# Performance work log

Hardware: AMD Instinct MI355X
Metric: run time of the kernel (lower is better)

Reference implementation:

```python
import jax, jax.numpy as jnp
import numpy as np

N_NODES = 50000
N_EDGES = 800000
IN_DIM = 256
HID = 64
HEADS = [4, 4, 1]
N_CLASSES = 16
SLOPE = 0.2


def mish(x):
    return x * jnp.tanh(jax.nn.softplus(x))


def gat_conv(x, src, dst, W, attn_l, attn_r, bias, res_W, n_heads, d_out, act):
    """DGL GATConv (feat_drop=attn_drop=0, residual=True, bias=True).
    x: (N, F_in); src/dst: (E,) edge endpoints; message flows src -> dst.
    """
    N = x.shape[0]
    feat = (x @ W).reshape(N, n_heads, d_out)            # (N, H, D)
    el = jnp.sum(feat * attn_l, axis=-1)                 # (N, H)
    er = jnp.sum(feat * attn_r, axis=-1)                 # (N, H)
    e = jax.nn.leaky_relu(el[src] + er[dst], SLOPE)      # (E, H)
    # segment softmax over incoming edges of each dst node
    emax = jax.ops.segment_max(e, dst, num_segments=N)   # (N, H)
    ee = jnp.exp(e - emax[dst])                          # (E, H)
    denom = jax.ops.segment_sum(ee, dst, num_segments=N) # (N, H)
    a = ee / denom[dst]                                  # (E, H)
    # weighted scatter-aggregate of source features
    rst = jax.ops.segment_sum(feat[src] * a[:, :, None], dst, num_segments=N)  # (N, H, D)
    # residual: identity if F_in == H*D else linear projection (DGL semantics)
    if res_W is None:
        res = x.reshape(N, n_heads, d_out)
    else:
        res = (x @ res_W).reshape(N, n_heads, d_out)
    rst = rst + res + bias.reshape(1, n_heads, d_out)
    if act:
        rst = mish(rst)
    return rst


def setup_inputs() -> dict:
    key = jax.random.key(0)
    ks = jax.random.split(key, 16)
    x = jax.random.normal(ks[0], (N_NODES, IN_DIM), dtype=jnp.float32)
    src = jax.random.randint(ks[1], (N_EDGES,), 0, N_NODES, dtype=jnp.int32)
    dst = jax.random.randint(ks[2], (N_EDGES,), 0, N_NODES, dtype=jnp.int32)
    s = 0.1
    # layer 0: 256 -> 4 heads x 64
    W0 = jax.random.normal(ks[3], (IN_DIM, HEADS[0] * HID), jnp.float32) * s
    al0 = jax.random.normal(ks[4], (HEADS[0], HID), jnp.float32) * s
    ar0 = jax.random.normal(ks[5], (HEADS[0], HID), jnp.float32) * s
    b0 = jnp.zeros((HEADS[0] * HID,), jnp.float32)
    # layer 1: 256 -> 4 heads x 64
    W1 = jax.random.normal(ks[6], (HEADS[0] * HID, HEADS[1] * HID), jnp.float32) * s
    al1 = jax.random.normal(ks[7], (HEADS[1], HID), jnp.float32) * s
    ar1 = jax.random.normal(ks[8], (HEADS[1], HID), jnp.float32) * s
    b1 = jnp.zeros((HEADS[1] * HID,), jnp.float32)
    # output layer: 256 -> 1 head x 16 (residual needs a linear projection)
    W2 = jax.random.normal(ks[9], (HEADS[1] * HID, HEADS[2] * N_CLASSES), jnp.float32) * s
    al2 = jax.random.normal(ks[10], (HEADS[2], N_CLASSES), jnp.float32) * s
    ar2 = jax.random.normal(ks[11], (HEADS[2], N_CLASSES), jnp.float32) * s
    b2 = jnp.zeros((HEADS[2] * N_CLASSES,), jnp.float32)
    resW2 = jax.random.normal(ks[12], (HEADS[1] * HID, HEADS[2] * N_CLASSES), jnp.float32) * s
    return {"x": x, "src": src, "dst": dst,
            "W0": W0, "al0": al0, "ar0": ar0, "b0": b0,
            "W1": W1, "al1": al1, "ar1": ar1, "b1": b1,
            "W2": W2, "al2": al2, "ar2": ar2, "b2": b2, "resW2": resW2}


def reference(x, src, dst, W0, al0, ar0, b0, W1, al1, ar1, b1, W2, al2, ar2, b2, resW2):
    N = x.shape[0]
    h = gat_conv(x, src, dst, W0, al0, ar0, b0, None, HEADS[0], HID, True).reshape(N, -1)
    h = gat_conv(h, src, dst, W1, al1, ar1, b1, None, HEADS[1], HID, True).reshape(N, -1)
    logits = gat_conv(h, src, dst, W2, al2, ar2, b2, resW2, HEADS[2], N_CLASSES, False).mean(axis=1)
    return logits
```

## Files before the change

### kernel.cpp

```cpp
#include <hip/hip_runtime.h>
#include <cmath>
#include <type_traits>

typedef __bf16 bf16;
typedef __attribute__((ext_vector_type(8))) __bf16 bf16x8;
typedef __attribute__((ext_vector_type(4))) __bf16 bf16x4;
typedef __attribute__((ext_vector_type(4))) float f32x4;

__device__ __forceinline__ unsigned f2s(float x) {
    unsigned u = __float_as_uint(x);
    return (u & 0x80000000u) ? ~u : (u | 0x80000000u);
}
__device__ __forceinline__ float s2f(unsigned s) {
    return (s & 0x80000000u) ? __uint_as_float(s & 0x7FFFFFFFu)
                             : __uint_as_float(~s);
}

__device__ __forceinline__ float fast_mish(float x) {
    const float t = __expf(fminf(x, 32.f));
    const float num = fmaf(t, t, t + t);
    const float den = num + 2.f;
    return x * num * __builtin_amdgcn_rcpf(den);
}

__global__ void prep_weights_kernel(const float* __restrict__ W0, const float* __restrict__ W1,
                                    const float* __restrict__ W2, const float* __restrict__ rW2,
                                    bf16* __restrict__ Wt0, bf16* __restrict__ Wt1,
                                    bf16* __restrict__ Bct) {
    const int idx = blockIdx.x * blockDim.x + threadIdx.x;
    if (idx < 65536) {
        const int k = idx >> 8, m = idx & 255;
        Wt0[m * 256 + k] = (bf16)W0[idx];
        Wt1[m * 256 + k] = (bf16)W1[idx];
    }
    if (idx < 8192) {
        const int m = idx >> 8, k = idx & 255;
        const float v = (m < 16) ? W2[k * 16 + m] : rW2[k * 16 + (m - 16)];
        Bct[idx] = (bf16)v;
    }
}

template <typename AT>
__global__ __launch_bounds__(256) void gemm_mfma_bf16(const AT* __restrict__ A,
                                                      const bf16* __restrict__ Bt,
                                                      bf16* __restrict__ Fb, int N) {
    constexpr int K = 256, BM = 128, BK = 32;
    constexpr int LDA = BK + 8;
    __shared__ bf16 As[BM * LDA];
    __shared__ bf16 Bs[BM * LDA];

    const int tid = threadIdx.x;
    const int wave = tid >> 6, lane = tid & 63;
    const int quad = lane >> 4, l16 = lane & 15;
    const int rowBase = blockIdx.y * BM;
    const int colBase = blockIdx.x * BM;
    const int m_base = (wave >> 1) * 64, n_base = (wave & 1) * 64;

    f32x4 acc[4][4] = {};

    const int sr = tid >> 1;
    const int seg = (tid & 1) << 4;

    for (int k0 = 0; k0 < K; k0 += BK) {
        {
            const int gr = rowBase + sr;
            if constexpr (std::is_same<AT, float>::value) {
                float4 f0 = {0,0,0,0}, f1 = {0,0,0,0}, f2 = {0,0,0,0}, f3 = {0,0,0,0};
                if (gr < N) {
                    const float4* Ag = (const float4*)(A + (long)gr * K + k0 + seg);
                    f0 = Ag[0]; f1 = Ag[1]; f2 = Ag[2]; f3 = Ag[3];
                }
                bf16x8 p0, p1;
                p0[0] = (bf16)f0.x; p0[1] = (bf16)f0.y; p0[2] = (bf16)f0.z; p0[3] = (bf16)f0.w;
                p0[4] = (bf16)f1.x; p0[5] = (bf16)f1.y; p0[6] = (bf16)f1.z; p0[7] = (bf16)f1.w;
                p1[0] = (bf16)f2.x; p1[1] = (bf16)f2.y; p1[2] = (bf16)f2.z; p1[3] = (bf16)f2.w;
                p1[4] = (bf16)f3.x; p1[5] = (bf16)f3.y; p1[6] = (bf16)f3.z; p1[7] = (bf16)f3.w;
                *(bf16x8*)&As[sr * LDA + seg] = p0;
                *(bf16x8*)&As[sr * LDA + seg + 8] = p1;
            } else {
                bf16x8 p0 = {}, p1 = {};
                if (gr < N) {
                    const bf16x8* Ag = (const bf16x8*)(A + (long)gr * K + k0 + seg);
                    p0 = Ag[0]; p1 = Ag[1];
                }
                *(bf16x8*)&As[sr * LDA + seg] = p0;
                *(bf16x8*)&As[sr * LDA + seg + 8] = p1;
            }
        }
        {
            const bf16x8* Bg = (const bf16x8*)(Bt + (long)(colBase + sr) * K + k0 + seg);
            *(bf16x8*)&Bs[sr * LDA + seg] = Bg[0];
            *(bf16x8*)&Bs[sr * LDA + seg + 8] = Bg[1];
        }
        __syncthreads();

        bf16x8 af[4], bfr[4];
#pragma unroll
        for (int mi = 0; mi < 4; mi++)
            af[mi] = *(const bf16x8*)&As[(m_base + mi * 16 + l16) * LDA + quad * 8];
#pragma unroll
        for (int ni = 0; ni < 4; ni++)
            bfr[ni] = *(const bf16x8*)&Bs[(n_base + ni * 16 + l16) * LDA + quad * 8];
#pragma unroll
        for (int mi = 0; mi < 4; mi++)
#pragma unroll
            for (int ni = 0; ni < 4; ni++)
                acc[mi][ni] = __builtin_amdgcn_mfma_f32_16x16x32_bf16(af[mi], bfr[ni], acc[mi][ni], 0, 0, 0);
        __syncthreads();
    }

#pragma unroll
    for (int mi = 0; mi < 4; mi++) {
#pragma unroll
        for (int r = 0; r < 4; r++) {
            const int grow = rowBase + m_base + mi * 16 + quad * 4 + r;
            if (grow < N) {
#pragma unroll
                for (int ni = 0; ni < 4; ni++) {
                    Fb[(long)grow * 256 + colBase + n_base + ni * 16 + l16] = (bf16)acc[mi][ni][r];
                }
            }
        }
    }
}

__global__ __launch_bounds__(256) void gemm_mfma_n32(const bf16* __restrict__ A,
                                                     const bf16* __restrict__ Bt,
                                                     float* __restrict__ C, int N) {
    constexpr int K = 256, BM = 128, BK = 32;
    constexpr int LDA = BK + 8;
    __shared__ bf16 As[BM * LDA];
    __shared__ bf16 Bs[32 * LDA];

    const int tid = threadIdx.x;
    const int wave = tid >> 6, lane = tid & 63;
    const int quad = lane >> 4, l16 = lane & 15;
    const int rowBase = blockIdx.x * BM;
    const int m_base = (wave >> 1) * 64, n_base = (wave & 1) * 16;

    f32x4 acc[4] = {};

    const int sr = tid >> 1;
    const int seg = (tid & 1) << 4;

    for (int k0 = 0; k0 < K; k0 += BK) {
        {
            const int gr = rowBase + sr;
            bf16x8 p0 = {}, p1 = {};
            if (gr < N) {
                const bf16x8* Ag = (const bf16x8*)(A + (long)gr * K + k0 + seg);
                p0 = Ag[0]; p1 = Ag[1];
            }
            *(bf16x8*)&As[sr * LDA + seg] = p0;
            *(bf16x8*)&As[sr * LDA + seg + 8] = p1;
        }
        if (tid < 64) {
            const int br = tid >> 1;
            const bf16x8* Bg = (const bf16x8*)(Bt + br * K + k0 + seg);
            *(bf16x8*)&Bs[br * LDA + seg] = Bg[0];
            *(bf16x8*)&Bs[br * LDA + seg + 8] = Bg[1];
        }
        __syncthreads();

        const bf16x8 bfr = *(const bf16x8*)&Bs[(n_base + l16) * LDA + quad * 8];
#pragma unroll
        for (int mi = 0; mi < 4; mi++) {
            const bf16x8 af = *(const bf16x8*)&As[(m_base + mi * 16 + l16) * LDA + quad * 8];
            acc[mi] = __builtin_amdgcn_mfma_f32_16x16x32_bf16(af, bfr, acc[mi], 0, 0, 0);
        }
        __syncthreads();
    }

#pragma unroll
    for (int mi = 0; mi < 4; mi++) {
#pragma unroll
        for (int r = 0; r < 4; r++) {
            const int grow = rowBase + m_base + mi * 16 + quad * 4 + r;
            if (grow < N) C[(long)grow * 32 + n_base + l16] = acc[mi][r];
        }
    }
}

__global__ void el_er_node_kernel(const bf16* __restrict__ feat,
                                  const float* __restrict__ al, const float* __restrict__ ar,
                                  float* __restrict__ el, float* __restrict__ er, int N) {
    const int wid = (blockIdx.x * blockDim.x + threadIdx.x) >> 6;
    const int lane = threadIdx.x & 63;
    if (wid >= N) return;
    const bf16x4 f = ((const bf16x4*)feat)[(long)wid * 64 + lane];
    const float4 a = ((const float4*)al)[lane];
    const float4 b = ((const float4*)ar)[lane];
    const float f0 = (float)f[0], f1 = (float)f[1], f2 = (float)f[2], f3 = (float)f[3];
    float vl = f0 * a.x + f1 * a.y + f2 * a.z + f3 * a.w;
    float vr = f0 * b.x + f1 * b.y + f2 * b.z + f3 * b.w;
#pragma unroll
    for (int off = 1; off < 16; off <<= 1) {
        vl += __shfl_xor(vl, off);
        vr += __shfl_xor(vr, off);
    }
    if ((lane & 15) == 0) {
        const int h = lane >> 4;
        el[wid * 4 + h] = vl;
        er[wid * 4 + h] = vr;
    }
}

__global__ void el_er_strided16(const float* __restrict__ feat, int stride,
                                const float* __restrict__ al, const float* __restrict__ ar,
                                float* __restrict__ el, float* __restrict__ er, int N) {
    const int wid = (blockIdx.x * blockDim.x + threadIdx.x) >> 6;
    const int lane = threadIdx.x & 63;
    if (wid >= N) return;
    float vl = 0.f, vr = 0.f;
    if (lane < 16) {
        float f = feat[(long)wid * stride + lane];
        vl = f * al[lane];
        vr = f * ar[lane];
    }
#pragma unroll
    for (int off = 1; off < 16; off <<= 1) {
        vl += __shfl_xor(vl, off);
        vr += __shfl_xor(vr, off);
    }
    if (lane == 0) { el[wid] = vl; er[wid] = vr; }
}

__global__ void elmax4_kernel(const float4* __restrict__ el4, unsigned* __restrict__ elmax_u, int n4) {
    __shared__ float4 sm[256];
    float4 m = {-INFINITY, -INFINITY, -INFINITY, -INFINITY};
    for (int i = blockIdx.x * blockDim.x + threadIdx.x; i < n4; i += gridDim.x * blockDim.x) {
        const float4 v = el4[i];
        m.x = fmaxf(m.x, v.x); m.y = fmaxf(m.y, v.y);
        m.z = fmaxf(m.z, v.z); m.w = fmaxf(m.w, v.w);
    }
    sm[threadIdx.x] = m;
    __syncthreads();
    for (int off = 128; off > 0; off >>= 1) {
        if (threadIdx.x < off) {
            float4 o = sm[threadIdx.x + off];
            float4 c = sm[threadIdx.x];
            c.x = fmaxf(c.x, o.x); c.y = fmaxf(c.y, o.y);
            c.z = fmaxf(c.z, o.z); c.w = fmaxf(c.w, o.w);
            sm[threadIdx.x] = c;
        }
        __syncthreads();
    }
    if (threadIdx.x == 0) {
        const float4 r = sm[0];
        atomicMax(&elmax_u[0], f2s(r.x));
        atomicMax(&elmax_u[1], f2s(r.y));
        atomicMax(&elmax_u[2], f2s(r.z));
        atomicMax(&elmax_u[3], f2s(r.w));
    }
}


__global__ void count_deg_kernel(const int* __restrict__ dst, int* __restrict__ deg, int E) {
    const int e = blockIdx.x * blockDim.x + threadIdx.x;
    if (e >= E) return;
    atomicAdd(&deg[dst[e]], 1);
}

__global__ void scan_block_kernel(const int* __restrict__ deg, int* __restrict__ scanned,
                                  int* __restrict__ block_sums, int N) {
    __shared__ int smem[256];
    const int tid = threadIdx.x;
    const int base = blockIdx.x * 1024 + tid * 4;
    int v[4];
#pragma unroll
    for (int i = 0; i < 4; i++) v[i] = (base + i < N) ? deg[base + i] : 0;
    const int tsum = v[0] + v[1] + v[2] + v[3];
    smem[tid] = tsum;
    __syncthreads();
    int acc = tsum;
    for (int off = 1; off < 256; off <<= 1) {
        const int t = (tid >= off) ? smem[tid - off] : 0;
        __syncthreads();
        acc += t;
        smem[tid] = acc;
        __syncthreads();
    }
    if (tid == 255) block_sums[blockIdx.x] = acc;
    int run = acc - tsum;
#pragma unroll
    for (int i = 0; i < 4; i++) {
        if (base + i < N) scanned[base + i] = run;
        run += v[i];
    }
}

__global__ void scan_sums_kernel(int* __restrict__ block_sums, unsigned* __restrict__ elmax_u, int nb) {
    const int tid = threadIdx.x;
    if (tid < 12) elmax_u[tid] = f2s(-INFINITY);
    const int orig = (tid < nb) ? block_sums[tid] : 0;
    int v = orig;
#pragma unroll
    for (int off = 1; off < 64; off <<= 1) {
        const int t = __shfl_up(v, off);
        if (tid >= off) v += t;
    }
    if (tid < nb) block_sums[tid] = v - orig;
}

__global__ void apply_offsets_kernel(const int* __restrict__ scanned, const int* __restrict__ block_sums,
                                     int* __restrict__ row_ptr, int* __restrict__ cursor, int N, int E) {
    const int i = blockIdx.x * blockDim.x + threadIdx.x;
    if (i < N) {
        const int v = scanned[i] + block_sums[i >> 10];
        row_ptr[i] = v;
        cursor[i] = v;
    }
    if (i == 0) row_ptr[N] = E;
}

__global__ void scatter_kernel(const int* __restrict__ src, const int* __restrict__ dst,
                               int* __restrict__ cursor, int* __restrict__ csr_src, int E) {
    const int e = blockIdx.x * blockDim.x + threadIdx.x;
    if (e >= E) return;
    const int pos = atomicAdd(&cursor[dst[e]], 1);
    csr_src[pos] = src[e];
}

template <int H, int D, bool ACT, typename RT, typename OT>
__global__ void gat_aggregate_wave(const int* __restrict__ row_ptr, const int* __restrict__ csr_src,
                                   const float* __restrict__ el, const float* __restrict__ er,
                                   const unsigned* __restrict__ elmax_u,
                                   const bf16* __restrict__ feat,
                                   const RT* __restrict__ res, const float* __restrict__ bias,
                                   OT* __restrict__ out, int N) {
    static_assert(H == 4 && D == 64, "layout hardcoded for C=256");
    const int wave = threadIdx.x >> 6;
    const int lane = threadIdx.x & 63;
    int n = blockIdx.x * (blockDim.x >> 6) + wave;
    if (n >= N) return;
    n = __builtin_amdgcn_readfirstlane(n);
    const int sel = lane >> 5;
    const int hl = lane & 31;
    const int h = hl >> 3;

    const float erd = er[n * H + h];
    float sh = s2f(elmax_u[h]) + erd;
    sh = fmaxf(sh, 0.2f * sh);
    constexpr float L2E = 1.4426950408889634f;
    const float C1 = (erd - sh) * L2E;
    const float C2 = fmaf(0.2f, erd, -sh) * L2E;

    const char* csrB = (const char*)csr_src;
    const char* elB = (const char*)el;
    const char* featB = (const char*)feat;
    const unsigned hoff = (unsigned)(h << 2);
    const unsigned coff = (unsigned)(hl << 4);
    const unsigned selo = (unsigned)(sel << 2);

    float acc[8] = {0.f, 0.f, 0.f, 0.f, 0.f, 0.f, 0.f, 0.f};
    float l = 0.f;
    int p = row_ptr[n];
    const int pend = row_ptr[n + 1];

#define CSRLD(PP) (*(const int*)(csrB + ((unsigned)((PP) << 2) + selo)))
#define ELLD(S)   (*(const float*)(elB + ((unsigned)((S) << 4) + hoff)))
#define FTLD(S)   (*(const bf16x8*)(featB + ((unsigned)((S) << 9) + coff)))
#define WCOMP(EV) __builtin_amdgcn_exp2f(fmaxf(fmaf((EV), L2E, C1), fmaf((EV), 0.2f * L2E, C2)))

    for (; p + 8 <= pend; p += 8) {
        const int sA = CSRLD(p);
        const int sB = CSRLD(p + 2);
        const int sC = CSRLD(p + 4);
        const int sD = CSRLD(p + 6);
        const float eA = ELLD(sA);
        const float eB = ELLD(sB);
        const float eC = ELLD(sC);
        const float eD = ELLD(sD);
        const bf16x8 fA = FTLD(sA);
        const bf16x8 fB = FTLD(sB);
        const bf16x8 fC = FTLD(sC);
        const bf16x8 fD = FTLD(sD);
        const float wA = WCOMP(eA);
        const float wB = WCOMP(eB);
        const float wC = WCOMP(eC);
        const float wD = WCOMP(eD);
        l += (wA + wB) + (wC + wD);
#pragma unroll
        for (int i = 0; i < 8; i++)
            acc[i] = fmaf(wA, (float)fA[i],
                     fmaf(wB, (float)fB[i],
                     fmaf(wC, (float)fC[i],
                     fmaf(wD, (float)fD[i], acc[i]))));
    }
    for (; p + 4 <= pend; p += 4) {
        const int sA = CSRLD(p);
        const int sB = CSRLD(p + 2);
        const float eA = ELLD(sA);
        const float eB = ELLD(sB);
        const bf16x8 fA = FTLD(sA);
        const bf16x8 fB = FTLD(sB);
        const float wA = WCOMP(eA);
        const float wB = WCOMP(eB);
        l += wA + wB;
#pragma unroll
        for (int i = 0; i < 8; i++)
            acc[i] = fmaf(wA, (float)fA[i], fmaf(wB, (float)fB[i], acc[i]));
    }
    for (; p + 2 <= pend; p += 2) {
        const int sA = CSRLD(p);
        const float eA = ELLD(sA);
        const bf16x8 fA = FTLD(sA);
        const float wA = WCOMP(eA);
        l += wA;
#pragma unroll
        for (int i = 0; i < 8; i++)
            acc[i] = fmaf(wA, (float)fA[i], acc[i]);
    }
    if (p < pend) {
        const int s_ = *(const int*)(csrB + (unsigned)(p << 2));
        const float ev_ = ELLD(s_);
        float w_ = WCOMP(ev_);
        if (sel) w_ = 0.f;
        const bf16x8 f_ = FTLD(s_);
        l += w_;
#pragma unroll
        for (int i_ = 0; i_ < 8; i_++) acc[i_] = fmaf(w_, (float)f_[i_], acc[i_]);
    }
#undef CSRLD
#undef ELLD
#undef FTLD
#undef WCOMP

    l += __shfl_xor(l, 32);
#pragma unroll
    for (int i = 0; i < 8; i++) acc[i] += __shfl_xor(acc[i], 32);
    const float inv = (l > 0.f) ? __builtin_amdgcn_rcpf(l) : 0.f;

    const float a0 = (sel ? acc[4] : acc[0]) * inv;
    const float a1 = (sel ? acc[5] : acc[1]) * inv;
    const float a2 = (sel ? acc[6] : acc[2]) * inv;
    const float a3 = (sel ? acc[7] : acc[3]) * inv;
    const unsigned ib = (unsigned)(sel << 2);

    float4 r;
    if constexpr (std::is_same<RT, float>::value) {
        r = *(const float4*)((const char*)res + ((size_t)n << 10) + (coff << 1) + (ib << 2));
    } else {
        const bf16x4 rb = *(const bf16x4*)((const char*)res + ((size_t)n << 9) + coff + (ib << 1));
        r = make_float4((float)rb[0], (float)rb[1], (float)rb[2], (float)rb[3]);
    }
    const float4 bb = *(const float4*)((const char*)bias + (coff << 1) + (ib << 2));
    float v0 = a0 + r.x + bb.x;
    float v1 = a1 + r.y + bb.y;
    float v2 = a2 + r.z + bb.z;
    float v3 = a3 + r.w + bb.w;
    if (ACT) {
        v0 = fast_mish(v0);
        v1 = fast_mish(v1);
        v2 = fast_mish(v2);
        v3 = fast_mish(v3);
    }
    if constexpr (std::is_same<OT, float>::value) {
        float4 o = {v0, v1, v2, v3};
        *(float4*)((char*)out + ((size_t)n << 10) + (coff << 1) + (ib << 2)) = o;
    } else {
        bf16x4 o;
        o[0] = (bf16)v0; o[1] = (bf16)v1; o[2] = (bf16)v2; o[3] = (bf16)v3;
        *(bf16x4*)((char*)out + ((size_t)n << 9) + coff + (ib << 1)) = o;
    }
}

__global__ void gat_aggregate_small16(const int* __restrict__ row_ptr, const int* __restrict__ csr_src,
                                      const float* __restrict__ el, const float* __restrict__ er,
                                      const unsigned* __restrict__ elmax_u,
                                      const float* __restrict__ F2, const float* __restrict__ bias,
                                      float* __restrict__ out, int N) {
    const int wave = threadIdx.x >> 6;
    const int lane = threadIdx.x & 63;
    int n = blockIdx.x * (blockDim.x >> 6) + wave;
    if (n >= N) return;
    n = __builtin_amdgcn_readfirstlane(n);
    const int slot = lane >> 4;
    const int c = lane & 15;

    const float mx = fmaxf(fmaxf(s2f(elmax_u[8]), s2f(elmax_u[9])),
                           fmaxf(s2f(elmax_u[10]), s2f(elmax_u[11])));
    const float erd = er[n];
    float sh = mx + erd;
    sh = fmaxf(sh, 0.2f * sh);
    constexpr float L2E = 1.4426950408889634f;
    const float C1 = (erd - sh) * L2E;
    const float C2 = fmaf(0.2f, erd, -sh) * L2E;

    const char* csrB = (const char*)csr_src;
    const char* elB = (const char*)el;
    const char* fB = (const char*)F2;
    const unsigned co = (unsigned)(c << 2);
    const unsigned so = (unsigned)(slot << 2);

    float acc = 0.f, l = 0.f;
    int p = row_ptr[n];
    const int pend = row_ptr[n + 1];
    for (; p + 8 <= pend; p += 8) {
        const int s0 = *(const int*)(csrB + ((unsigned)(p << 2) + so));
        const int s1 = *(const int*)(csrB + ((unsigned)((p + 4) << 2) + so));
        const float e0 = *(const float*)(elB + (unsigned)(s0 << 2));
        const float e1 = *(const float*)(elB + (unsigned)(s1 << 2));
        const float f0 = *(const float*)(fB + ((unsigned)(s0 << 7) + co));
        const float f1 = *(const float*)(fB + ((unsigned)(s1 << 7) + co));
        const float w0 = __builtin_amdgcn_exp2f(
            fmaxf(fmaf(e0, L2E, C1), fmaf(e0, 0.2f * L2E, C2)));
        const float w1 = __builtin_amdgcn_exp2f(
            fmaxf(fmaf(e1, L2E, C1), fmaf(e1, 0.2f * L2E, C2)));
        l += w0 + w1;
        acc = fmaf(w0, f0, fmaf(w1, f1, acc));
    }
    for (; p + 4 <= pend; p += 4) {
        const int s_ = *(const int*)(csrB + ((unsigned)(p << 2) + so));
        const float ev_ = *(const float*)(elB + (unsigned)(s_ << 2));
        const float w_ = __builtin_amdgcn_exp2f(
            fmaxf(fmaf(ev_, L2E, C1), fmaf(ev_, 0.2f * L2E, C2)));
        const float f_ = *(const float*)(fB + ((unsigned)(s_ << 7) + co));
        l += w_;
        acc = fmaf(w_, f_, acc);
    }
    if (p < pend) {
        const int q = p + slot;
        const bool valid = q < pend;
        const int qi = valid ? q : p;
        const int s_ = *(const int*)(csrB + (unsigned)(qi << 2));
        const float ev_ = *(const float*)(elB + (unsigned)(s_ << 2));
        float w_ = __builtin_amdgcn_exp2f(
            fmaxf(fmaf(ev_, L2E, C1), fmaf(ev_, 0.2f * L2E, C2)));
        if (!valid) w_ = 0.f;
        const float f_ = *(const float*)(fB + ((unsigned)(s_ << 7) + co));
        l += w_;
        acc = fmaf(w_, f_, acc);
    }
    l += __shfl_xor(l, 16);
    l += __shfl_xor(l, 32);
    acc += __shfl_xor(acc, 16);
    acc += __shfl_xor(acc, 32);
    const float inv = (l > 0.f) ? __builtin_amdgcn_rcpf(l) : 0.f;
    if (lane < 16) {
        const float rv = *(const float*)(fB + ((unsigned)(n << 7) + 64u + co));
        out[(long)n * 16 + c] = fmaf(acc, inv, rv + bias[c]);
    }
}


static inline int cdiv(long a, long b) { return (int)((a + b - 1) / b); }

extern "C" void kernel_launch(void* const* d_in, const int* in_sizes, int n_in,
                              void* d_out, int out_size, void* d_ws, size_t ws_size,
                              hipStream_t stream) {
    const float* x   = (const float*)d_in[0];
    const int*   src = (const int*)d_in[1];
    const int*   dst = (const int*)d_in[2];
    const float* W0  = (const float*)d_in[3];
    const float* al0 = (const float*)d_in[4];
    const float* ar0 = (const float*)d_in[5];
    const float* b0  = (const float*)d_in[6];
    const float* W1  = (const float*)d_in[7];
    const float* al1 = (const float*)d_in[8];
    const float* ar1 = (const float*)d_in[9];
    const float* b1  = (const float*)d_in[10];
    const float* W2  = (const float*)d_in[11];
    const float* al2 = (const float*)d_in[12];
    const float* ar2 = (const float*)d_in[13];
    const float* b2  = (const float*)d_in[14];
    const float* rW2 = (const float*)d_in[15];
    float* out = (float*)d_out;

    const int N = in_sizes[0] / 256;
    const int E = in_sizes[1];

    bf16* Wt0    = (bf16*)d_ws;
    bf16* Wt1    = Wt0 + 65536;
    bf16* Bct    = Wt1 + 65536;
    bf16* Fb     = Bct + 8192;
    bf16* Hb     = Fb + (long)N * 256;
    float* F2    = (float*)(Hb + (long)N * 256);
    float* el    = F2 + (long)N * 32;
    float* er    = el + (long)N * 4;
    unsigned* elmax_u = (unsigned*)(er + (long)N * 4);
    int* deg     = (int*)(elmax_u + 12);
    int* scanned = deg + N;
    int* bsums   = scanned + N;
    int* row_ptr = bsums + 64;
    int* cursor  = row_ptr + N + 1;
    int* csr_src = cursor + N;

    const int THREADS = 256;
    const int NB = cdiv(N, 1024);
    dim3 mfma_grid(2, cdiv(N, 128));

    prep_weights_kernel<<<cdiv(65536, THREADS), THREADS, 0, stream>>>(W0, W1, W2, rW2, Wt0, Wt1, Bct);
    hipMemsetAsync(deg, 0, (size_t)N * 4, stream);
    count_deg_kernel<<<cdiv(E, THREADS), THREADS, 0, stream>>>(dst, deg, E);
    scan_block_kernel<<<NB, 256, 0, stream>>>(deg, scanned, bsums, N);
    scan_sums_kernel<<<1, 64, 0, stream>>>(bsums, elmax_u, NB);
    apply_offsets_kernel<<<cdiv(N, THREADS), THREADS, 0, stream>>>(scanned, bsums, row_ptr, cursor, N, E);
    scatter_kernel<<<cdiv(E, THREADS), THREADS, 0, stream>>>(src, dst, cursor, csr_src, E);

    gemm_mfma_bf16<float><<<mfma_grid, 256, 0, stream>>>(x, Wt0, Fb, N);
    el_er_node_kernel<<<cdiv(N, 4), 256, 0, stream>>>(Fb, al0, ar0, el, er, N);
    elmax4_kernel<<<64, 256, 0, stream>>>((const float4*)el, elmax_u, N);
    gat_aggregate_wave<4, 64, true, float, bf16><<<cdiv(N, 4), 256, 0, stream>>>(
        row_ptr, csr_src, el, er, elmax_u, Fb, x, b0, Hb, N);

    gemm_mfma_bf16<bf16><<<mfma_grid, 256, 0, stream>>>(Hb, Wt1, Fb, N);
    el_er_node_kernel<<<cdiv(N, 4), 256, 0, stream>>>(Fb, al1, ar1, el, er, N);
    elmax4_kernel<<<64, 256, 0, stream>>>((const float4*)el, elmax_u + 4, N);
    gat_aggregate_wave<4, 64, true, bf16, bf16><<<cdiv(N, 4), 256, 0, stream>>>(
        row_ptr, csr_src, el, er, elmax_u + 4, Fb, Hb, b1, Hb, N);

    gemm_mfma_n32<<<cdiv(N, 128), 256, 0, stream>>>(Hb, Bct, F2, N);
    el_er_strided16<<<cdiv(N, 4), 256, 0, stream>>>(F2, 32, al2, ar2, el, er, N);
    elmax4_kernel<<<64, 256, 0, stream>>>((const float4*)el, elmax_u + 8, N / 4);
    gat_aggregate_small16<<<cdiv(N, 4), 256, 0, stream>>>(row_ptr, csr_src, el, er, elmax_u,
                                                          F2, b2, out, N);
}
```

Before: 447.8 us.

## Split output-layer features into separate arrays and precompute CSR slot positions

The last-layer GEMM now writes the projected features and the residual projection into two separate 16-wide float arrays instead of one interleaved 32-wide array. The gather in the final aggregation then reads from a compact 64-byte row, which halves the cache lines it touches per random source node. In the CSR build, the degree-count atomic now records each edge's slot within its destination. The scatter step computes the write position from row_ptr plus that slot, removing the second atomic pass and the cursor array at the cost of an extra E-sized int buffer.

```diff
diff --git a/kernel.cpp b/kernel.cpp
--- a/kernel.cpp
+++ b/kernel.cpp
@@ -126,7 +126,8 @@
 
 __global__ __launch_bounds__(256) void gemm_mfma_n32(const bf16* __restrict__ A,
                                                      const bf16* __restrict__ Bt,
-                                                     float* __restrict__ C, int N) {
+                                                     float* __restrict__ F2f,
+                                                     float* __restrict__ F2r, int N) {
     constexpr int K = 256, BM = 128, BK = 32;
     constexpr int LDA = BK + 8;
     __shared__ bf16 As[BM * LDA];
@@ -171,12 +172,13 @@
         __syncthreads();
     }
 
+    float* __restrict__ Cq = (wave & 1) ? F2r : F2f;
 #pragma unroll
     for (int mi = 0; mi < 4; mi++) {
 #pragma unroll
         for (int r = 0; r < 4; r++) {
             const int grow = rowBase + m_base + mi * 16 + quad * 4 + r;
-            if (grow < N) C[(long)grow * 32 + n_base + l16] = acc[mi][r];
+            if (grow < N) Cq[(long)grow * 16 + l16] = acc[mi][r];
         }
     }
 }
@@ -254,11 +256,11 @@
     }
 }
 
-
-__global__ void count_deg_kernel(const int* __restrict__ dst, int* __restrict__ deg, int E) {
+__global__ void count_deg_kernel(const int* __restrict__ dst, int* __restrict__ deg,
+                                 int* __restrict__ pos, int E) {
     const int e = blockIdx.x * blockDim.x + threadIdx.x;
     if (e >= E) return;
-    atomicAdd(&deg[dst[e]], 1);
+    pos[e] = atomicAdd(&deg[dst[e]], 1);
 }
 
 __global__ void scan_block_kernel(const int* __restrict__ deg, int* __restrict__ scanned,
@@ -303,22 +305,18 @@
 }
 
 __global__ void apply_offsets_kernel(const int* __restrict__ scanned, const int* __restrict__ block_sums,
-                                     int* __restrict__ row_ptr, int* __restrict__ cursor, int N, int E) {
+                                     int* __restrict__ row_ptr, int N, int E) {
     const int i = blockIdx.x * blockDim.x + threadIdx.x;
-    if (i < N) {
-        const int v = scanned[i] + block_sums[i >> 10];
-        row_ptr[i] = v;
-        cursor[i] = v;
-    }
+    if (i < N) row_ptr[i] = scanned[i] + block_sums[i >> 10];
     if (i == 0) row_ptr[N] = E;
 }
 
 __global__ void scatter_kernel(const int* __restrict__ src, const int* __restrict__ dst,
-                               int* __restrict__ cursor, int* __restrict__ csr_src, int E) {
+                               const int* __restrict__ row_ptr, const int* __restrict__ pos,
+                               int* __restrict__ csr_src, int E) {
     const int e = blockIdx.x * blockDim.x + threadIdx.x;
     if (e >= E) return;
-    const int pos = atomicAdd(&cursor[dst[e]], 1);
-    csr_src[pos] = src[e];
+    csr_src[row_ptr[dst[e]] + pos[e]] = src[e];
 }
 
 template <int H, int D, bool ACT, typename RT, typename OT>
@@ -468,7 +466,8 @@
 __global__ void gat_aggregate_small16(const int* __restrict__ row_ptr, const int* __restrict__ csr_src,
                                       const float* __restrict__ el, const float* __restrict__ er,
                                       const unsigned* __restrict__ elmax_u,
-                                      const float* __restrict__ F2, const float* __restrict__ bias,
+                                      const float* __restrict__ F2f, const float* __restrict__ F2r,
+                                      const float* __restrict__ bias,
                                       float* __restrict__ out, int N) {
     const int wave = threadIdx.x >> 6;
     const int lane = threadIdx.x & 63;
@@ -489,7 +488,7 @@
 
     const char* csrB = (const char*)csr_src;
     const char* elB = (const char*)el;
-    const char* fB = (const char*)F2;
+    const char* fB = (const char*)F2f;
     const unsigned co = (unsigned)(c << 2);
     const unsigned so = (unsigned)(slot << 2);
 
@@ -501,8 +500,8 @@
         const int s1 = *(const int*)(csrB + ((unsigned)((p + 4) << 2) + so));
         const float e0 = *(const float*)(elB + (unsigned)(s0 << 2));
         const float e1 = *(const float*)(elB + (unsigned)(s1 << 2));
-        const float f0 = *(const float*)(fB + ((unsigned)(s0 << 7) + co));
-        const float f1 = *(const float*)(fB + ((unsigned)(s1 << 7) + co));
+        const float f0 = *(const float*)(fB + ((unsigned)(s0 << 6) + co));
+        const float f1 = *(const float*)(fB + ((unsigned)(s1 << 6) + co));
         const float w0 = __builtin_amdgcn_exp2f(
             fmaxf(fmaf(e0, L2E, C1), fmaf(e0, 0.2f * L2E, C2)));
         const float w1 = __builtin_amdgcn_exp2f(
@@ -515,7 +514,7 @@
         const float ev_ = *(const float*)(elB + (unsigned)(s_ << 2));
         const float w_ = __builtin_amdgcn_exp2f(
             fmaxf(fmaf(ev_, L2E, C1), fmaf(ev_, 0.2f * L2E, C2)));
-        const float f_ = *(const float*)(fB + ((unsigned)(s_ << 7) + co));
+        const float f_ = *(const float*)(fB + ((unsigned)(s_ << 6) + co));
         l += w_;
         acc = fmaf(w_, f_, acc);
     }
@@ -528,7 +527,7 @@
         float w_ = __builtin_amdgcn_exp2f(
             fmaxf(fmaf(ev_, L2E, C1), fmaf(ev_, 0.2f * L2E, C2)));
         if (!valid) w_ = 0.f;
-        const float f_ = *(const float*)(fB + ((unsigned)(s_ << 7) + co));
+        const float f_ = *(const float*)(fB + ((unsigned)(s_ << 6) + co));
         l += w_;
         acc = fmaf(w_, f_, acc);
     }
@@ -538,7 +537,7 @@
     acc += __shfl_xor(acc, 32);
     const float inv = (l > 0.f) ? __builtin_amdgcn_rcpf(l) : 0.f;
     if (lane < 16) {
-        const float rv = *(const float*)(fB + ((unsigned)(n << 7) + 64u + co));
+        const float rv = F2r[(long)n * 16 + c];
         out[(long)n * 16 + c] = fmaf(acc, inv, rv + bias[c]);
     }
 }
@@ -575,16 +574,17 @@
     bf16* Bct    = Wt1 + 65536;
     bf16* Fb     = Bct + 8192;
     bf16* Hb     = Fb + (long)N * 256;
-    float* F2    = (float*)(Hb + (long)N * 256);
-    float* el    = F2 + (long)N * 32;
+    float* F2f   = (float*)(Hb + (long)N * 256);
+    float* F2r   = F2f + (long)N * 16;
+    float* el    = F2r + (long)N * 16;
     float* er    = el + (long)N * 4;
     unsigned* elmax_u = (unsigned*)(er + (long)N * 4);
     int* deg     = (int*)(elmax_u + 12);
     int* scanned = deg + N;
     int* bsums   = scanned + N;
     int* row_ptr = bsums + 64;
-    int* cursor  = row_ptr + N + 1;
-    int* csr_src = cursor + N;
+    int* pos     = row_ptr + N + 1;
+    int* csr_src = pos + E;
 
     const int THREADS = 256;
     const int NB = cdiv(N, 1024);
@@ -592,11 +592,11 @@
 
     prep_weights_kernel<<<cdiv(65536, THREADS), THREADS, 0, stream>>>(W0, W1, W2, rW2, Wt0, Wt1, Bct);
     hipMemsetAsync(deg, 0, (size_t)N * 4, stream);
-    count_deg_kernel<<<cdiv(E, THREADS), THREADS, 0, stream>>>(dst, deg, E);
+    count_deg_kernel<<<cdiv(E, THREADS), THREADS, 0, stream>>>(dst, deg, pos, E);
     scan_block_kernel<<<NB, 256, 0, stream>>>(deg, scanned, bsums, N);
     scan_sums_kernel<<<1, 64, 0, stream>>>(bsums, elmax_u, NB);
-    apply_offsets_kernel<<<cdiv(N, THREADS), THREADS, 0, stream>>>(scanned, bsums, row_ptr, cursor, N, E);
-    scatter_kernel<<<cdiv(E, THREADS), THREADS, 0, stream>>>(src, dst, cursor, csr_src, E);
+    apply_offsets_kernel<<<cdiv(N, THREADS), THREADS, 0, stream>>>(scanned, bsums, row_ptr, N, E);
+    scatter_kernel<<<cdiv(E, THREADS), THREADS, 0, stream>>>(src, dst, row_ptr, pos, csr_src, E);
 
     gemm_mfma_bf16<float><<<mfma_grid, 256, 0, stream>>>(x, Wt0, Fb, N);
     el_er_node_kernel<<<cdiv(N, 4), 256, 0, stream>>>(Fb, al0, ar0, el, er, N);
@@ -610,9 +610,9 @@
     gat_aggregate_wave<4, 64, true, bf16, bf16><<<cdiv(N, 4), 256, 0, stream>>>(
         row_ptr, csr_src, el, er, elmax_u + 4, Fb, Hb, b1, Hb, N);
 
-    gemm_mfma_n32<<<cdiv(N, 128), 256, 0, stream>>>(Hb, Bct, F2, N);
-    el_er_strided16<<<cdiv(N, 4), 256, 0, stream>>>(F2, 32, al2, ar2, el, er, N);
+    gemm_mfma_n32<<<cdiv(N, 128), 256, 0, stream>>>(Hb, Bct, F2f, F2r, N);
+    el_er_strided16<<<cdiv(N, 4), 256, 0, stream>>>(F2f, 16, al2, ar2, el, er, N);
     elmax4_kernel<<<64, 256, 0, stream>>>((const float4*)el, elmax_u + 8, N / 4);
     gat_aggregate_small16<<<cdiv(N, 4), 256, 0, stream>>>(row_ptr, csr_src, el, er, elmax_u,
-                                                          F2, b2, out, N);
-}
+                                                          F2f, F2r, b2, out, N);
+}
```

Result: faster. 417.3 us (-6.8%).
